# Kernel optimization log

Measured on AMD Instinct MI355X. Metric: run time of the kernel, lower is better.

Reference implementation:

```python
import jax, jax.numpy as jnp
import numpy as np

B, T, D, L = 8, 8192, 256, 3
DISTS = (1, 5, 15, 30)


def _layernorm(x, g, b, eps=1e-5):
    m = x.mean(-1, keepdims=True)
    v = ((x - m) ** 2).mean(-1, keepdims=True)
    return (x - m) * jax.lax.rsqrt(v + eps) * g + b


def _temporal_edges():
    src, dst = [], []
    for d in DISTS:
        a = np.arange(T - d)
        src += [a, a + d]
        dst += [a + d, a]
    ei = np.stack([np.concatenate(src), np.concatenate(dst)])  # [2, E]
    off = (np.arange(B) * T).repeat(ei.shape[1])
    return np.tile(ei, (1, B)) + off[None, :]  # [2, B*E]


def setup_inputs() -> dict:
    key = jax.random.key(0)
    ks = jax.random.split(key, 6)
    s = 1.0 / np.sqrt(D)
    s4 = 1.0 / np.sqrt(4 * D)
    return dict(
        x=jax.random.normal(ks[0], (B, T, D), jnp.float32),
        adjacency=jnp.zeros((T, T), jnp.float32),  # shape-check only
        edge_index=jnp.asarray(_temporal_edges(), jnp.int32),
        conv_w=jax.random.normal(ks[1], (L, D, D), jnp.float32) * s,
        conv_b=jnp.zeros((L, D), jnp.float32),
        norm_g=jnp.ones((L, D), jnp.float32),
        norm_b=jnp.zeros((L, D), jnp.float32),
        normff_g=jnp.ones((D,), jnp.float32),
        normff_b=jnp.zeros((D,), jnp.float32),
        w1=jax.random.normal(ks[2], (D, 4 * D), jnp.float32) * s,
        b1=jnp.zeros((4 * D,), jnp.float32),
        w2=jax.random.normal(ks[3], (4 * D, D), jnp.float32) * s4,
        b2=jnp.zeros((D,), jnp.float32),
    )


def reference(x, adjacency, edge_index, conv_w, conv_b, norm_g, norm_b,
              normff_g, normff_b, w1, b1, w2, b2):
    b, t, d = x.shape
    n = b * t
    xf = x.reshape(n, d)
    src, dst = edge_index[0], edge_index[1]
    # GCN symmetric degree normalization (no self loops), degrees by target node
    deg = jax.ops.segment_sum(jnp.ones(src.shape[0], x.dtype), dst, num_segments=n)
    dinv = jnp.where(deg > 0, jax.lax.rsqrt(deg), 0.0)
    enorm = (dinv[src] * dinv[dst])[:, None]  # [E,1]
    for i in range(conv_w.shape[0]):
        h = xf @ conv_w[i]                                    # [N,D]
        h = jax.ops.segment_sum(h[src] * enorm, dst, num_segments=n) + conv_b[i]
        h = jax.nn.gelu(h, approximate=False)
        h = _layernorm(h.reshape(b, t, d), norm_g[i], norm_b[i]).reshape(n, d)
        xf = xf + h
    x = xf.reshape(b, t, d)
    y = _layernorm(x, normff_g, normff_b)
    ff = jax.nn.gelu(y @ w1 + b1, approximate=False) @ w2 + b2
    return x + ff
```

## Files before the change

### kernel.cpp

```cpp
#include <hip/hip_runtime.h>
#include <hip/hip_bf16.h>
#include <math.h>
#include <stdint.h>
#include <stddef.h>

#define TB 8
#define TT 8192
#define DD 256
#define NR (TB * TT)
#define HH 1024
#define LL 3

typedef unsigned short ushort_t;
typedef __attribute__((ext_vector_type(8))) short short8;
typedef __attribute__((ext_vector_type(4))) float floatx4;

__device__ __forceinline__ float bf2f(ushort_t u) {
  union { unsigned int i; float f; } x; x.i = ((unsigned int)u) << 16; return x.f;
}
__device__ __forceinline__ ushort_t f2bf(float f) {
  union { float f; unsigned int i; } x; x.f = f;
  unsigned int r = x.i + 0x7fffu + ((x.i >> 16) & 1u);
  return (ushort_t)(r >> 16);
}
__device__ __forceinline__ float ld_in(const void* p, size_t i, int isf) {
  return isf ? ((const float*)p)[i] : bf2f(((const ushort_t*)p)[i]);
}
__device__ __forceinline__ float gelu_f(float v) {
  const float y = v * (0.7978845608028654f + 0.035677408136300125f * v * v);
  const float e = __expf(-2.0f * y);
  return v * __builtin_amdgcn_rcpf(1.0f + e);
}
__device__ __forceinline__ int deg_of(int t) {
  return (t >= 1) + (t >= 5) + (t >= 15) + (t >= 30)
       + (t < TT - 1) + (t < TT - 5) + (t < TT - 15) + (t < TT - 30);
}
__device__ __forceinline__ void gl_lds16(const ushort_t* g, void* l) {
  __builtin_amdgcn_global_load_lds(
      (const __attribute__((address_space(1))) unsigned int*)(g),
      (__attribute__((address_space(3))) unsigned int*)(l), 16, 0, 0);
}
__device__ __forceinline__ int xcd_swz(int lin, int nwg) {
  const int q = nwg >> 3;
  return (lin & 7) * q + (lin >> 3);
}
__device__ __forceinline__ int swz128(int row, int bytecol) {
  return row * 128 + (bytecol ^ ((row & 7) << 4));
}
__device__ __forceinline__ int swz64(int row, int bytecol) {
  return row * 64 + (bytecol ^ ((row & 3) << 4));
}
#define WAIT_VM0()  asm volatile("s_waitcnt vmcnt(0)" ::: "memory")
#define WAIT_LGKM0() asm volatile("s_waitcnt lgkmcnt(0)" ::: "memory")

__global__ void k_probe(const void* __restrict__ x, int* __restrict__ flag) {
  if (threadIdx.x == 0 && blockIdx.x == 0) {
    const float* fb = (const float*)x;
    int okf = 0;
    for (int i = 0; i < 128; ++i) {
      const float av = fabsf(fb[i]);
      if (av > 1e-6f && av < 100.f) okf++;
    }
    *flag = (okf >= 115) ? 1 : 0;
  }
}

__device__ __forceinline__ void transpose_tile(
    char* smem_, const void* cw, const void* w1, const void* w2,
    ushort_t* cwT, ushort_t* w1T, ushort_t* w2T, int isf, int b, int tid) {
  ushort_t (*tile)[33] = (ushort_t(*)[33])smem_;
  const void* src; ushort_t* dst; int R, C, bx, by; size_t row0;
  if (b < 192) {
    const int i = b >> 6, t = b & 63;
    src = cw; dst = cwT + (size_t)i * DD * DD; row0 = (size_t)i * DD;
    R = DD; C = DD; bx = (t & 7) * 32; by = (t >> 3) * 32;
  } else if (b < 448) {
    const int t = b - 192;
    src = w1; dst = w1T; row0 = 0; R = DD; C = HH;
    bx = (t & 31) * 32; by = (t >> 5) * 32;
  } else {
    const int t = b - 448;
    src = w2; dst = w2T; row0 = 0; R = HH; C = DD;
    bx = (t & 7) * 32; by = (t >> 3) * 32;
  }
  const int tx = tid & 31, ty = tid >> 5;
  __syncthreads();
  for (int i = ty; i < 32; i += 8)
    tile[i][tx] = f2bf(ld_in(src, (row0 + by + i) * (size_t)C + bx + tx, isf));
  __syncthreads();
  for (int i = ty; i < 32; i += 8)
    dst[(size_t)(bx + i) * R + by + tx] = tile[tx][i];
}

__global__ __launch_bounds__(256) void k_phase0(
    const void* __restrict__ x, ushort_t* __restrict__ xA,
    const void* __restrict__ cw, const void* __restrict__ w1,
    const void* __restrict__ w2, ushort_t* __restrict__ cwT,
    ushort_t* __restrict__ w1T, ushort_t* __restrict__ w2T,
    const int* __restrict__ flag) {
  __shared__ alignas(16) char smem[4224];
  const int isf = *flag;
  const int bid = blockIdx.x, tid = threadIdx.x;
  transpose_tile(smem, cw, w1, w2, cwT, w1T, w2T, isf, bid, tid);
  if (bid < 192)
    transpose_tile(smem, cw, w1, w2, cwT, w1T, w2T, isf, 512 + bid, tid);
  const size_t c0 = (size_t)bid * 8192 + tid;
  if (isf) {
    const float4* xf = (const float4*)x;
    ushort4* xo = (ushort4*)xA;
#pragma unroll
    for (int i = 0; i < 32; ++i) {
      const float4 f = xf[c0 + i * 256];
      ushort4 u; u.x = f2bf(f.x); u.y = f2bf(f.y); u.z = f2bf(f.z); u.w = f2bf(f.w);
      xo[c0 + i * 256] = u;
    }
  } else {
#pragma unroll
    for (int i = 0; i < 32; ++i)
      ((ushort4*)xA)[c0 + i * 256] = ((const ushort4*)x)[c0 + i * 256];
  }
}

__global__ __launch_bounds__(256, 2) void k_conv_fused(
    const ushort_t* __restrict__ xin, ushort_t* __restrict__ xout,
    const ushort_t* __restrict__ Bt, const void* __restrict__ bias,
    size_t boff, const void* __restrict__ g, const void* __restrict__ bn,
    size_t goff, const int* __restrict__ flag) {
  __shared__ alignas(16) char smem[68096];
  float* scr    = (float*)smem;
  float* part   = scr;
  float* partsq = scr + 256;
  float* smu    = scr + 512;
  float* srs    = scr + 576;
  char* aggA    = smem + 2560;
  char* rt      = smem + 2560;
  const int isf = *flag;

  const int tid  = threadIdx.x;
  const int lane = tid & 63;
  const int l16  = lane & 15;
  const int quad = lane >> 4;
  const int w    = tid >> 6;
  const int m0   = xcd_swz(blockIdx.x, gridDim.x) * 64;

  char* lB = smem + 35328 + w * 8192;

  const int srow = lane >> 3;
  const int sseg = (lane & 7) ^ (srow & 7);
  auto stageB = [&](int kc) {
#pragma unroll
    for (int i = 0; i < 8; ++i)
      gl_lds16(Bt + (size_t)(w * 64 + i * 8 + srow) * DD + kc * 64 + sseg * 8,
               lB + i * 1024);
  };
  stageB(0);

  const int tbase = m0 & (TT - 1);
  const bool interior = (tbase >= 60) && (tbase <= TT - 124);
  const int koffs[8] = {-30, -15, -5, -1, 1, 5, 15, 30};
#pragma unroll
  for (int j = 0; j < 8; ++j) {
    const int id = j * 256 + tid;
    const int r = id >> 5, c = id & 31;
    const ushort_t* base = xin + (size_t)(m0 + r) * DD + c * 8;
    float s[8] = {0.f, 0.f, 0.f, 0.f, 0.f, 0.f, 0.f, 0.f};
    if (interior) {
#pragma unroll
      for (int e = 0; e < 8; ++e) {
        const short8 u = *(const short8*)(base + (ptrdiff_t)koffs[e] * DD);
#pragma unroll
        for (int q2 = 0; q2 < 8; ++q2) s[q2] += bf2f((ushort_t)u[q2]);
      }
#pragma unroll
      for (int q2 = 0; q2 < 8; ++q2) s[q2] *= 0.125f;
    } else {
      const int t = tbase + r;
      const float di = rsqrtf((float)deg_of(t));
#pragma unroll
      for (int e = 0; e < 8; ++e) {
        const int t2 = t + koffs[e];
        if ((unsigned)t2 < (unsigned)TT) {
          const float wgt = di * rsqrtf((float)deg_of(t2));
          const short8 u = *(const short8*)(base + (ptrdiff_t)koffs[e] * DD);
#pragma unroll
          for (int q2 = 0; q2 < 8; ++q2) s[q2] += wgt * bf2f((ushort_t)u[q2]);
        }
      }
    }
    short8 o;
#pragma unroll
    for (int q2 = 0; q2 < 8; ++q2) o[q2] = (short)f2bf(s[q2]);
    *(short8*)(aggA + (c >> 3) * 8192 + swz128(r, (c & 7) * 16)) = o;
  }
  WAIT_LGKM0();
  __builtin_amdgcn_s_barrier();
  __builtin_amdgcn_sched_barrier(0);

  floatx4 acc[4][4];
#pragma unroll
  for (int i = 0; i < 4; ++i)
#pragma unroll
    for (int j = 0; j < 4; ++j) acc[i][j] = {0.f, 0.f, 0.f, 0.f};

#pragma unroll
  for (int kc = 0; kc < 4; ++kc) {
    WAIT_VM0();
    short8 af0[4], bf0[4], af1[4], bf1[4];
#pragma unroll
    for (int mt = 0; mt < 4; ++mt) {
      af0[mt] = *(const short8*)(aggA + kc * 8192 +
                   swz128(mt * 16 + l16, quad * 16));
      af1[mt] = *(const short8*)(aggA + kc * 8192 +
                   swz128(mt * 16 + l16, 64 + quad * 16));
    }
#pragma unroll
    for (int nt = 0; nt < 4; ++nt) {
      bf0[nt] = *(const short8*)(lB + swz128(nt * 16 + l16, quad * 16));
      bf1[nt] = *(const short8*)(lB + swz128(nt * 16 + l16, 64 + quad * 16));
    }
    WAIT_LGKM0();
    __builtin_amdgcn_sched_barrier(0);
    if (kc < 3) stageB(kc + 1);
#pragma unroll
    for (int mt = 0; mt < 4; ++mt)
#pragma unroll
      for (int nt = 0; nt < 4; ++nt)
        acc[mt][nt] = __builtin_amdgcn_mfma_f32_16x16x32_bf16(
            af0[mt], bf0[nt], acc[mt][nt], 0, 0, 0);
#pragma unroll
    for (int mt = 0; mt < 4; ++mt)
#pragma unroll
      for (int nt = 0; nt < 4; ++nt)
        acc[mt][nt] = __builtin_amdgcn_mfma_f32_16x16x32_bf16(
            af1[mt], bf1[nt], acc[mt][nt], 0, 0, 0);
  }

#pragma unroll
  for (int nt = 0; nt < 4; ++nt) {
    const float bv = ld_in(bias, boff + w * 64 + nt * 16 + l16, isf);
#pragma unroll
    for (int mt = 0; mt < 4; ++mt)
#pragma unroll
      for (int r = 0; r < 4; ++r)
        acc[mt][nt][r] = gelu_f(acc[mt][nt][r] + bv);
  }
#pragma unroll
  for (int mt = 0; mt < 4; ++mt) {
#pragma unroll
    for (int r = 0; r < 4; ++r) {
      float p = 0.f, q = 0.f;
#pragma unroll
      for (int nt = 0; nt < 4; ++nt) {
        const float v = acc[mt][nt][r];
        p += v; q += v * v;
      }
#pragma unroll
      for (int o = 8; o > 0; o >>= 1) {
        p += __shfl_xor(p, o, 64);
        q += __shfl_xor(q, o, 64);
      }
      if (l16 == 0) {
        const int rowloc = mt * 16 + quad * 4 + r;
        part[w * 64 + rowloc] = p;
        partsq[w * 64 + rowloc] = q;
      }
    }
  }
  __syncthreads();
  if (tid < 64) {
    const float s  = part[tid] + part[64 + tid] + part[128 + tid] + part[192 + tid];
    const float sq = partsq[tid] + partsq[64 + tid] + partsq[128 + tid] + partsq[192 + tid];
    const float mu = s * (1.0f / DD);
    const float var = sq * (1.0f / DD) - mu * mu;
    smu[tid] = mu;
    srs[tid] = rsqrtf(var + 1e-5f);
  }
  __syncthreads();

#pragma unroll
  for (int nt = 0; nt < 4; ++nt) {
    const int col = w * 64 + nt * 16 + l16;
    const float gv = ld_in(g, goff + col, isf);
    const float bnv = ld_in(bn, goff + col, isf);
#pragma unroll
    for (int mt = 0; mt < 4; ++mt) {
#pragma unroll
      for (int r = 0; r < 4; ++r) {
        const int rowloc = mt * 16 + quad * 4 + r;
        *(ushort_t*)(rt + (rowloc * 264 + col) * 2) =
            f2bf((acc[mt][nt][r] - smu[rowloc]) * srs[rowloc] * gv + bnv);
      }
    }
  }
  __syncthreads();

#pragma unroll
  for (int i = 0; i < 8; ++i) {
    const int ch = tid + i * 256;
    const int row = ch >> 5, sg = ch & 31;
    const short8 xv = *(const short8*)(xin + (size_t)(m0 + row) * DD + sg * 8);
    const short8 rv = *(const short8*)(rt + (row * 264 + sg * 8) * 2);
    short8 ov;
#pragma unroll
    for (int j = 0; j < 8; ++j)
      ov[j] = (short)f2bf(bf2f((ushort_t)xv[j]) + bf2f((ushort_t)rv[j]));
    *(short8*)(xout + (size_t)(m0 + row) * DD + sg * 8) = ov;
  }
}

__global__ __launch_bounds__(256, 2) void k_ffn(
    const ushort_t* __restrict__ xb, const ushort_t* __restrict__ w1T,
    const ushort_t* __restrict__ w2T, const void* __restrict__ gff,
    const void* __restrict__ bff, const void* __restrict__ b1,
    const void* __restrict__ b2, void* __restrict__ dout,
    const int* __restrict__ flag) {
  __shared__ alignas(16) char smem[65536];
  char* An = smem;
  char* Zs = smem + 32768;
  char* Rs = smem;
  const int isf = *flag;

  const int tid  = threadIdx.x;
  const int lane = tid & 63;
  const int l16  = lane & 15;
  const int quad = lane >> 4;
  const int w    = tid >> 6;
  const int m0   = xcd_swz(blockIdx.x, gridDim.x) * 64;
  char* Bw = smem + 49152 + w * 4096;

  const int sr8 = lane >> 3;
  const int ss8 = (lane & 7) ^ (sr8 & 7);
  auto stageB1 = [&](int n1, int kc) {
#pragma unroll
    for (int i = 0; i < 4; ++i)
      gl_lds16(w1T + (size_t)(n1 * 128 + w * 32 + i * 8 + sr8) * DD +
                   kc * 64 + ss8 * 8,
               Bw + i * 1024);
  };
  const int sr4 = lane >> 2;
  const int ss4 = (lane & 3) ^ (sr4 & 3);
  auto stageB2 = [&](int n1, int kc2, int ks) {
#pragma unroll
    for (int i = 0; i < 4; ++i)
      gl_lds16(w2T + (size_t)(w * 64 + i * 16 + sr4) * HH +
                   n1 * 128 + kc2 * 64 + ks * 32 + ss4 * 8,
               Bw + i * 1024);
  };

  stageB1(0, 0);

  const int sg = tid & 31;
  float gffv[8], bffv[8];
#pragma unroll
  for (int j = 0; j < 8; ++j) {
    gffv[j] = ld_in(gff, sg * 8 + j, isf);
    bffv[j] = ld_in(bff, sg * 8 + j, isf);
  }
#pragma unroll
  for (int i = 0; i < 8; ++i) {
    const int row = (tid + i * 256) >> 5;
    const short8 xv = *(const short8*)(xb + (size_t)(m0 + row) * DD + sg * 8);
    float v[8], ps = 0.f, pq = 0.f;
#pragma unroll
    for (int j = 0; j < 8; ++j) {
      v[j] = bf2f((ushort_t)xv[j]); ps += v[j]; pq += v[j] * v[j];
    }
#pragma unroll
    for (int o = 16; o > 0; o >>= 1) {
      ps += __shfl_xor(ps, o, 64);
      pq += __shfl_xor(pq, o, 64);
    }
    const float mu = ps * (1.0f / DD);
    const float rs = rsqrtf(pq * (1.0f / DD) - mu * mu + 1e-5f);
    short8 o8;
#pragma unroll
    for (int j = 0; j < 8; ++j)
      o8[j] = (short)f2bf((v[j] - mu) * rs * gffv[j] + bffv[j]);
    *(short8*)(An + (sg >> 3) * 8192 + swz128(row, (sg & 7) * 16)) = o8;
  }
  WAIT_LGKM0();
  __builtin_amdgcn_s_barrier();
  __builtin_amdgcn_sched_barrier(0);

  floatx4 acc2[4][4];
#pragma unroll
  for (int i = 0; i < 4; ++i)
#pragma unroll
    for (int j = 0; j < 4; ++j) acc2[i][j] = {0.f, 0.f, 0.f, 0.f};

  for (int n1 = 0; n1 < 8; ++n1) {
    floatx4 acc1[4][2];
#pragma unroll
    for (int i = 0; i < 4; ++i)
#pragma unroll
      for (int j = 0; j < 2; ++j) acc1[i][j] = {0.f, 0.f, 0.f, 0.f};

#pragma unroll
    for (int kc = 0; kc < 4; ++kc) {
      WAIT_VM0();
      short8 af0[4], af1[4], bq0[2], bq1[2];
#pragma unroll
      for (int mt = 0; mt < 4; ++mt)
        af0[mt] = *(const short8*)(An + kc * 8192 +
                     swz128(mt * 16 + l16, quad * 16));
#pragma unroll
      for (int nt = 0; nt < 2; ++nt)
        bq0[nt] = *(const short8*)(Bw + swz128(nt * 16 + l16, quad * 16));
#pragma unroll
      for (int mt = 0; mt < 4; ++mt)
#pragma unroll
        for (int nt = 0; nt < 2; ++nt)
          acc1[mt][nt] = __builtin_amdgcn_mfma_f32_16x16x32_bf16(
              af0[mt], bq0[nt], acc1[mt][nt], 0, 0, 0);
#pragma unroll
      for (int mt = 0; mt < 4; ++mt)
        af1[mt] = *(const short8*)(An + kc * 8192 +
                     swz128(mt * 16 + l16, 64 + quad * 16));
#pragma unroll
      for (int nt = 0; nt < 2; ++nt)
        bq1[nt] = *(const short8*)(Bw + swz128(nt * 16 + l16, 64 + quad * 16));
      WAIT_LGKM0();
      __builtin_amdgcn_sched_barrier(0);
      if (kc < 3) stageB1(n1, kc + 1);
#pragma unroll
      for (int mt = 0; mt < 4; ++mt)
#pragma unroll
        for (int nt = 0; nt < 2; ++nt)
          acc1[mt][nt] = __builtin_amdgcn_mfma_f32_16x16x32_bf16(
              af1[mt], bq1[nt], acc1[mt][nt], 0, 0, 0);
    }

#pragma unroll
    for (int nt = 0; nt < 2; ++nt) {
      const int col = w * 32 + nt * 16 + l16;
      const float b1v = ld_in(b1, n1 * 128 + col, isf);
#pragma unroll
      for (int mt = 0; mt < 4; ++mt)
#pragma unroll
        for (int r = 0; r < 4; ++r) {
          const int row = mt * 16 + quad * 4 + r;
          *(ushort_t*)(Zs + (col >> 6) * 8192 + swz128(row, (col & 63) * 2)) =
              f2bf(gelu_f(acc1[mt][nt][r] + b1v));
        }
    }
    stageB2(n1, 0, 0);
    WAIT_LGKM0();
    __builtin_amdgcn_s_barrier();
    __builtin_amdgcn_sched_barrier(0);

#pragma unroll
    for (int kc2 = 0; kc2 < 2; ++kc2) {
#pragma unroll
      for (int ks = 0; ks < 2; ++ks) {
        WAIT_VM0();
        short8 af[4], bfr[4];
#pragma unroll
        for (int mt = 0; mt < 4; ++mt)
          af[mt] = *(const short8*)(Zs + kc2 * 8192 +
                     swz128(mt * 16 + l16, ks * 64 + quad * 16));
#pragma unroll
        for (int nt = 0; nt < 4; ++nt)
          bfr[nt] = *(const short8*)(Bw + swz64(nt * 16 + l16, quad * 16));
        WAIT_LGKM0();
        __builtin_amdgcn_sched_barrier(0);
        if (kc2 == 0 || ks == 0) stageB2(n1, kc2 + (ks & 1), (ks + 1) & 1);
        else if (n1 < 7) stageB1(n1 + 1, 0);
#pragma unroll
        for (int mt = 0; mt < 4; ++mt)
#pragma unroll
          for (int nt = 0; nt < 4; ++nt)
            acc2[mt][nt] = __builtin_amdgcn_mfma_f32_16x16x32_bf16(
                af[mt], bfr[nt], acc2[mt][nt], 0, 0, 0);
      }
    }
    __builtin_amdgcn_s_barrier();
    __builtin_amdgcn_sched_barrier(0);
  }

  WAIT_VM0();
#pragma unroll
  for (int i = 0; i < 8; ++i)
    gl_lds16(xb + (size_t)(m0 + ((i * 256 + tid) >> 5)) * DD +
                 ((i * 256 + tid) & 31) * 8,
             Rs + i * 4096 + w * 1024);
  __syncthreads();

#pragma unroll
  for (int nt = 0; nt < 4; ++nt) {
    const int col = w * 64 + nt * 16 + l16;
    const float b2v = ld_in(b2, col, isf);
#pragma unroll
    for (int mt = 0; mt < 4; ++mt) {
#pragma unroll
      for (int r = 0; r < 4; ++r) {
        const int lr = mt * 16 + quad * 4 + r;
        const float v = acc2[mt][nt][r] + b2v +
                        bf2f(*(const ushort_t*)(Rs + lr * 512 + col * 2));
        const size_t idx = (size_t)(m0 + lr) * DD + col;
        if (isf) ((float*)dout)[idx] = v;
        else     ((ushort_t*)dout)[idx] = f2bf(v);
      }
    }
  }
}

extern "C" void kernel_launch(void* const* d_in, const int* in_sizes, int n_in,
                              void* d_out, int out_size, void* d_ws, size_t ws_size,
                              hipStream_t stream) {
  const void* x      = d_in[0];
  const void* conv_w = d_in[3];
  const void* conv_b = d_in[4];
  const void* norm_g = d_in[5];
  const void* norm_b = d_in[6];
  const void* nff_g  = d_in[7];
  const void* nff_b  = d_in[8];
  const void* w1     = d_in[9];
  const void* b1     = d_in[10];
  const void* w2     = d_in[11];
  const void* b2     = d_in[12];
  (void)in_sizes; (void)n_in; (void)out_size; (void)ws_size;

  char* ws = (char*)d_ws;
  int*      flag = (int*)ws;      ws += 16;
  ushort_t* xA   = (ushort_t*)ws; ws += (size_t)NR * DD * 2;
  ushort_t* xB   = (ushort_t*)ws; ws += (size_t)NR * DD * 2;
  ushort_t* cwT  = (ushort_t*)ws; ws += (size_t)LL * DD * DD * 2;
  ushort_t* w1T  = (ushort_t*)ws; ws += (size_t)DD * HH * 2;
  ushort_t* w2T  = (ushort_t*)ws; ws += (size_t)HH * DD * 2;

  k_probe<<<1, 64, 0, stream>>>(x, flag);
  k_phase0<<<512, 256, 0, stream>>>(x, xA, conv_w, w1, w2, cwT, w1T, w2T,
                                    flag);

  k_conv_fused<<<NR / 64, 256, 0, stream>>>(
      xA, xB, cwT, conv_b, 0, norm_g, norm_b, 0, flag);
  k_conv_fused<<<NR / 64, 256, 0, stream>>>(
      xB, xA, cwT + (size_t)DD * DD, conv_b, DD, norm_g, norm_b, DD, flag);
  k_conv_fused<<<NR / 64, 256, 0, stream>>>(
      xA, xB, cwT + (size_t)2 * DD * DD, conv_b, 2 * DD, norm_g, norm_b,
      2 * DD, flag);

  k_ffn<<<NR / 64, 256, 0, stream>>>(
      xB, w1T, w2T, nff_g, nff_b, b1, b2, d_out, flag);
}
```

Measured before the change: 644.5 us.

## Double-buffer FFN weight staging with two-deep global-to-LDS prefetch

```diff
diff --git a/kernel.cpp b/kernel.cpp
--- a/kernel.cpp
+++ b/kernel.cpp
@@ -51,6 +51,7 @@
   return row * 64 + (bytecol ^ ((row & 3) << 4));
 }
 #define WAIT_VM0()  asm volatile("s_waitcnt vmcnt(0)" ::: "memory")
+#define WAIT_VM4()  asm volatile("s_waitcnt vmcnt(4)" ::: "memory")
 #define WAIT_LGKM0() asm volatile("s_waitcnt lgkmcnt(0)" ::: "memory")
 
 __global__ void k_probe(const void* __restrict__ x, int* __restrict__ flag) {
@@ -314,7 +315,7 @@
     const void* __restrict__ bff, const void* __restrict__ b1,
     const void* __restrict__ b2, void* __restrict__ dout,
     const int* __restrict__ flag) {
-  __shared__ alignas(16) char smem[65536];
+  __shared__ alignas(16) char smem[81920];
   char* An = smem;
   char* Zs = smem + 32768;
   char* Rs = smem;
@@ -326,28 +327,35 @@
   const int quad = lane >> 4;
   const int w    = tid >> 6;
   const int m0   = xcd_swz(blockIdx.x, gridDim.x) * 64;
-  char* Bw = smem + 49152 + w * 4096;
+  char* Bw0 = smem + 49152 + w * 8192;
 
   const int sr8 = lane >> 3;
   const int ss8 = (lane & 7) ^ (sr8 & 7);
-  auto stageB1 = [&](int n1, int kc) {
-#pragma unroll
-    for (int i = 0; i < 4; ++i)
-      gl_lds16(w1T + (size_t)(n1 * 128 + w * 32 + i * 8 + sr8) * DD +
-                   kc * 64 + ss8 * 8,
-               Bw + i * 1024);
-  };
   const int sr4 = lane >> 2;
   const int ss4 = (lane & 3) ^ (sr4 & 3);
-  auto stageB2 = [&](int n1, int kc2, int ks) {
-#pragma unroll
-    for (int i = 0; i < 4; ++i)
-      gl_lds16(w2T + (size_t)(w * 64 + i * 16 + sr4) * HH +
-                   n1 * 128 + kc2 * 64 + ks * 32 + ss4 * 8,
-               Bw + i * 1024);
+
+  auto stage_g = [&](int gg) {
+    if (gg >= 64) return;
+    const int n1 = gg >> 3, s = gg & 7;
+    char* dst = Bw0 + (gg & 1) * 4096;
+    if (s < 4) {
+#pragma unroll
+      for (int i = 0; i < 4; ++i)
+        gl_lds16(w1T + (size_t)(n1 * 128 + w * 32 + i * 8 + sr8) * DD +
+                     s * 64 + ss8 * 8,
+                 dst + i * 1024);
+    } else {
+      const int kc2 = (s - 4) >> 1, ks = (s - 4) & 1;
+#pragma unroll
+      for (int i = 0; i < 4; ++i)
+        gl_lds16(w2T + (size_t)(w * 64 + i * 16 + sr4) * HH +
+                     n1 * 128 + kc2 * 64 + ks * 32 + ss4 * 8,
+                 dst + i * 1024);
+    }
   };
 
-  stageB1(0, 0);
+  stage_g(0);
+  stage_g(1);
 
   const int sg = tid & 31;
   float gffv[8], bffv[8];
@@ -389,6 +397,9 @@
     for (int j = 0; j < 4; ++j) acc2[i][j] = {0.f, 0.f, 0.f, 0.f};
 
   for (int n1 = 0; n1 < 8; ++n1) {
+    const float b1v0 = ld_in(b1, n1 * 128 + w * 32 + l16, isf);
+    const float b1v1 = ld_in(b1, n1 * 128 + w * 32 + 16 + l16, isf);
+
     floatx4 acc1[4][2];
 #pragma unroll
     for (int i = 0; i < 4; ++i)
@@ -397,15 +408,25 @@
 
 #pragma unroll
     for (int kc = 0; kc < 4; ++kc) {
-      WAIT_VM0();
+      const int gs = n1 * 8 + kc;
+      WAIT_VM4();
+      const char* Bw = Bw0 + (gs & 1) * 4096;
       short8 af0[4], af1[4], bq0[2], bq1[2];
 #pragma unroll
-      for (int mt = 0; mt < 4; ++mt)
+      for (int mt = 0; mt < 4; ++mt) {
         af0[mt] = *(const short8*)(An + kc * 8192 +
                      swz128(mt * 16 + l16, quad * 16));
-#pragma unroll
-      for (int nt = 0; nt < 2; ++nt)
+        af1[mt] = *(const short8*)(An + kc * 8192 +
+                     swz128(mt * 16 + l16, 64 + quad * 16));
+      }
+#pragma unroll
+      for (int nt = 0; nt < 2; ++nt) {
         bq0[nt] = *(const short8*)(Bw + swz128(nt * 16 + l16, quad * 16));
+        bq1[nt] = *(const short8*)(Bw + swz128(nt * 16 + l16, 64 + quad * 16));
+      }
+      WAIT_LGKM0();
+      __builtin_amdgcn_sched_barrier(0);
+      stage_g(gs + 2);
 #pragma unroll
       for (int mt = 0; mt < 4; ++mt)
 #pragma unroll
@@ -414,16 +435,6 @@
               af0[mt], bq0[nt], acc1[mt][nt], 0, 0, 0);
 #pragma unroll
       for (int mt = 0; mt < 4; ++mt)
-        af1[mt] = *(const short8*)(An + kc * 8192 +
-                     swz128(mt * 16 + l16, 64 + quad * 16));
-#pragma unroll
-      for (int nt = 0; nt < 2; ++nt)
-        bq1[nt] = *(const short8*)(Bw + swz128(nt * 16 + l16, 64 + quad * 16));
-      WAIT_LGKM0();
-      __builtin_amdgcn_sched_barrier(0);
-      if (kc < 3) stageB1(n1, kc + 1);
-#pragma unroll
-      for (int mt = 0; mt < 4; ++mt)
 #pragma unroll
         for (int nt = 0; nt < 2; ++nt)
           acc1[mt][nt] = __builtin_amdgcn_mfma_f32_16x16x32_bf16(
@@ -433,7 +444,7 @@
 #pragma unroll
     for (int nt = 0; nt < 2; ++nt) {
       const int col = w * 32 + nt * 16 + l16;
-      const float b1v = ld_in(b1, n1 * 128 + col, isf);
+      const float b1v = nt ? b1v1 : b1v0;
 #pragma unroll
       for (int mt = 0; mt < 4; ++mt)
 #pragma unroll
@@ -443,35 +454,33 @@
               f2bf(gelu_f(acc1[mt][nt][r] + b1v));
         }
     }
-    stageB2(n1, 0, 0);
     WAIT_LGKM0();
     __builtin_amdgcn_s_barrier();
     __builtin_amdgcn_sched_barrier(0);
 
 #pragma unroll
-    for (int kc2 = 0; kc2 < 2; ++kc2) {
-#pragma unroll
-      for (int ks = 0; ks < 2; ++ks) {
-        WAIT_VM0();
-        short8 af[4], bfr[4];
-#pragma unroll
-        for (int mt = 0; mt < 4; ++mt)
-          af[mt] = *(const short8*)(Zs + kc2 * 8192 +
-                     swz128(mt * 16 + l16, ks * 64 + quad * 16));
+    for (int s2 = 0; s2 < 4; ++s2) {
+      const int gs = n1 * 8 + 4 + s2;
+      const int kc2 = s2 >> 1, ks = s2 & 1;
+      if (gs == 63) { WAIT_VM0(); } else { WAIT_VM4(); }
+      const char* Bw = Bw0 + (gs & 1) * 4096;
+      short8 af[4], bfr[4];
+#pragma unroll
+      for (int mt = 0; mt < 4; ++mt)
+        af[mt] = *(const short8*)(Zs + kc2 * 8192 +
+                   swz128(mt * 16 + l16, ks * 64 + quad * 16));
+#pragma unroll
+      for (int nt = 0; nt < 4; ++nt)
+        bfr[nt] = *(const short8*)(Bw + swz64(nt * 16 + l16, quad * 16));
+      WAIT_LGKM0();
+      __builtin_amdgcn_sched_barrier(0);
+      stage_g(gs + 2);
+#pragma unroll
+      for (int mt = 0; mt < 4; ++mt)
 #pragma unroll
         for (int nt = 0; nt < 4; ++nt)
-          bfr[nt] = *(const short8*)(Bw + swz64(nt * 16 + l16, quad * 16));
-        WAIT_LGKM0();
-        __builtin_amdgcn_sched_barrier(0);
-        if (kc2 == 0 || ks == 0) stageB2(n1, kc2 + (ks & 1), (ks + 1) & 1);
-        else if (n1 < 7) stageB1(n1 + 1, 0);
-#pragma unroll
-        for (int mt = 0; mt < 4; ++mt)
-#pragma unroll
-          for (int nt = 0; nt < 4; ++nt)
-            acc2[mt][nt] = __builtin_amdgcn_mfma_f32_16x16x32_bf16(
-                af[mt], bfr[nt], acc2[mt][nt], 0, 0, 0);
-      }
+          acc2[mt][nt] = __builtin_amdgcn_mfma_f32_16x16x32_bf16(
+              af[mt], bfr[nt], acc2[mt][nt], 0, 0, 0);
     }
     __builtin_amdgcn_s_barrier();
     __builtin_amdgcn_sched_barrier(0);
```

Measured after the change: 628.0 us (median of 2 runs). 2.6% less time.
